# Performance work log

Hardware: AMD Instinct MI355X
Metric: run time of the kernel (lower is better)

Reference implementation:

```python
import jax, jax.numpy as jnp
import numpy as np
import math

T = 1024      # num tokens
D = 1024      # hidden_size
H = 16        # attention heads
KV = 4        # kv heads
DH = 64       # head_dim
E = 8         # routed experts
K = 2         # top-k
F = 512       # moe_intermediate_size
FS = 2048     # shared_expert_intermediate_size
L = 2         # layers
V = 4096      # codec vocab
THETA = 1e6
EPS = 1e-6


def rms(x, w):
    return x * jax.lax.rsqrt(jnp.mean(x * x, -1, keepdims=True) + EPS) * w


def rope(x, pos):
    # x: [T, h, DH], rotate-half (non-interleaved) rotary
    half = DH // 2
    inv = 1.0 / (THETA ** (jnp.arange(half, dtype=jnp.float32) / half))
    ang = pos.astype(jnp.float32)[:, None] * inv          # [T, half]
    cos = jnp.concatenate([jnp.cos(ang)] * 2, -1)[:, None, :]
    sin = jnp.concatenate([jnp.sin(ang)] * 2, -1)[:, None, :]
    rot = jnp.concatenate([-x[..., half:], x[..., :half]], -1)
    return x * cos + rot * sin


def setup_inputs() -> dict:
    key = jax.random.key(0)
    ks = jax.random.split(key, 20)
    s = 0.02
    n = lambda k, shp: jax.random.normal(k, shp, dtype=jnp.float32) * s
    return {
        "input_ids": jax.random.randint(ks[0], (T,), 0, V),
        "positions": jnp.arange(T),
        "emb": n(ks[1], (V, D)),
        "ln1": jnp.ones((L, D), jnp.float32),
        "wq": n(ks[2], (L, D, H * DH)),
        "wk": n(ks[3], (L, D, KV * DH)),
        "wv": n(ks[4], (L, D, KV * DH)),
        "wo": n(ks[5], (L, H * DH, D)),
        "qn": jnp.ones((L, DH), jnp.float32),
        "kn": jnp.ones((L, DH), jnp.float32),
        "ln2": jnp.ones((L, D), jnp.float32),
        "router_w": n(ks[6], (L, D, E)),
        "egu": n(ks[7], (L, E, D, 2 * F)),
        "edn": n(ks[8], (L, E, F, D)),
        "sgu": n(ks[9], (L, D, 2 * FS)),
        "sdn": n(ks[10], (L, FS, D)),
        "sg_gate": n(ks[11], (L, D)),
        "final_ln": jnp.ones((D,), jnp.float32),
    }


def forward(input_ids, positions, emb, ln1, wq, wk, wv, wo, qn, kn, ln2,
            router_w, egu, edn, sgu, sdn, sg_gate, final_ln):
    h = emb[input_ids]                          # [T, D]
    res = jnp.zeros_like(h)
    causal = jnp.tril(jnp.ones((T, T), bool))
    scale = 1.0 / math.sqrt(DH)
    for i in range(L):
        # --- attention (pre-norm, fused add-residual semantics) ---
        res = h + res
        hn = rms(res, ln1[i])
        q = rms((hn @ wq[i]).reshape(T, H, DH), qn[i])
        k = rms((hn @ wk[i]).reshape(T, KV, DH), kn[i])
        v = (hn @ wv[i]).reshape(T, KV, DH)
        q, k = rope(q, positions), rope(k, positions)
        k = jnp.repeat(k, H // KV, axis=1)      # GQA expand
        v = jnp.repeat(v, H // KV, axis=1)
        att = jnp.einsum('qhd,khd->hqk', q, k) * scale
        att = jnp.where(causal[None], att, -jnp.inf)
        att = jax.nn.softmax(att, axis=-1)
        o = jnp.einsum('hqk,khd->qhd', att, v).reshape(T, H * DH) @ wo[i]
        # --- MoE MLP with shared expert ---
        res = o + res
        hn = rms(res, ln2[i])
        # shared expert: SiluAndMul + down, gated by sigmoid scalar
        gu = hn @ sgu[i]
        shared = (jax.nn.silu(gu[:, :FS]) * gu[:, FS:]) @ sdn[i]
        shared = shared * jax.nn.sigmoid(hn @ sg_gate[i])[:, None]
        # routed experts: softmax router, top-k, renormalize
        probs = jax.nn.softmax(hn @ router_w[i], axis=-1)      # [T, E]
        w, idx = jax.lax.top_k(probs, K)
        w = w / jnp.sum(w, -1, keepdims=True)
        comb = jnp.zeros((T, E), hn.dtype).at[jnp.arange(T)[:, None], idx].add(w)
        g = jnp.einsum('td,edf->tef', hn, egu[i])              # [T, E, 2F]
        he = jax.nn.silu(g[..., :F]) * g[..., F:]              # [T, E, F]
        routed = jnp.einsum('tef,efd,te->td', he, edn[i], comb)
        h = routed + shared
    res = h + res
    return rms(res, final_ln)


def reference(input_ids, positions, emb, ln1, wq, wk, wv, wo, qn, kn, ln2,
              router_w, egu, edn, sgu, sdn, sg_gate, final_ln):
    return forward(input_ids, positions, emb, ln1, wq, wk, wv, wo, qn, kn, ln2,
                   router_w, egu, edn, sgu, sdn, sg_gate, final_ln)
```

## Files before the change

kernel.cpp:

```cpp
#include <hip/hip_runtime.h>
#include <hip/hip_bf16.h>

#define T_ 1024
#define D_ 1024
#define H_ 16
#define KV_ 4
#define DH_ 64
#define E_ 8
#define TOPK_ 2
#define F_ 512
#define FS_ 2048
#define L_ 2

typedef unsigned int uint32;
typedef __attribute__((ext_vector_type(8))) short short8;
typedef __attribute__((ext_vector_type(4))) short short4v;
typedef __attribute__((ext_vector_type(4))) float f32x4;

__device__ __forceinline__ short f2bf(float f){
  uint32 u = __float_as_uint(f);
  return (short)((u + 0x7fffu + ((u >> 16) & 1u)) >> 16);
}
__device__ __forceinline__ float bf2f(short s){
  return __uint_as_float(((uint32)(unsigned short)s) << 16);
}

__device__ __forceinline__ void split8(const float* src, short8& h8, short8& l8){
  #pragma unroll
  for (int j = 0; j < 8; j++){
    short hi = f2bf(src[j]);
    h8[j] = hi;
    l8[j] = f2bf(src[j] - bf2f(hi));
  }
}

__global__ void k_embed(const int* __restrict__ ids, const float* __restrict__ emb,
                        float* __restrict__ h, float* __restrict__ res){
  int idx = blockIdx.x * 256 + threadIdx.x;
  int t = idx >> 10, d = idx & 1023;
  h[idx] = emb[(size_t)ids[t] * D_ + d];
  res[idx] = 0.f;
}

__global__ void k_zero_i32(int* __restrict__ p, int n){
  int i = blockIdx.x * 64 + threadIdx.x;
  if (i < n) p[i] = 0;
}

__global__ __launch_bounds__(256)
void k_fused_rms(float* __restrict__ res, const float* __restrict__ h,
                 const float* __restrict__ w, float* __restrict__ out){
  int t = blockIdx.x, tid = threadIdx.x;
  float* rr = res + (size_t)t * D_;
  const float* hr = h + (size_t)t * D_;
  float ss = 0.f;
  float vloc[4];
  #pragma unroll
  for (int u = 0; u < 4; u++){
    int d = tid + u * 256;
    float v = rr[d] + hr[d];
    vloc[u] = v;
    ss += v * v;
  }
  #pragma unroll
  for (int o = 32; o; o >>= 1) ss += __shfl_xor(ss, o);
  __shared__ float red[4];
  if ((tid & 63) == 0) red[tid >> 6] = ss;
  __syncthreads();
  float r = rsqrtf((red[0] + red[1] + red[2] + red[3]) * (1.f / D_) + 1e-6f);
  float* orow = out + (size_t)t * D_;
  #pragma unroll
  for (int u = 0; u < 4; u++){
    int d = tid + u * 256;
    rr[d] = vloc[u];
    orow[d] = vloc[u] * r * w[d];
  }
}

__global__ __launch_bounds__(64)
void k_qknorm_rope(float* __restrict__ buf, const float* __restrict__ nw,
                   const int* __restrict__ pos, int nheads){
  int row = blockIdx.x;
  int t = row / nheads;
  int lane = threadIdx.x;
  int base = row * DH_ + lane;
  float x = buf[base];
  float ss = x * x;
  #pragma unroll
  for (int o = 32; o; o >>= 1) ss += __shfl_xor(ss, o);
  float r = rsqrtf(ss * (1.f / DH_) + 1e-6f);
  float xn = x * r * nw[lane];
  int j = lane & 31;
  float inv = powf(1.0e6f, -(float)j * (1.f / 32.f));
  float ang = (float)pos[t] * inv;
  float s, c;
  sincosf(ang, &s, &c);
  float p = __shfl_xor(xn, 32);
  float rot = (lane < 32) ? -p : p;
  buf[base] = xn * c + rot * s;
}

__global__ __launch_bounds__(256)
void k_fattn(const float* __restrict__ q, const float* __restrict__ k,
             const float* __restrict__ v, float* __restrict__ out){
  const int h = blockIdx.x, qt = blockIdx.y;
  const int kvh = h >> 2;
  const int tid = threadIdx.x;
  const int w = tid >> 6, lane = tid & 63, l16 = lane & 15, lq = lane >> 4;

  __shared__ __align__(16) short Kh[64][72], Kl[64][72];
  __shared__ __align__(16) short Vth[64][72], Vtl[64][72];
  __shared__ __align__(16) short Ph[64][72], Pl[64][72];

  short8 qh[2], ql[2];
  {
    const float* qp = q + ((size_t)(qt * 64 + w * 16 + l16) * H_ + h) * DH_;
    #pragma unroll
    for (int s = 0; s < 2; s++){
      float a8[8];
      *(float4*)&a8[0] = *(const float4*)(qp + lq * 8 + 32 * s);
      *(float4*)&a8[4] = *(const float4*)(qp + lq * 8 + 32 * s + 4);
      split8(a8, qh[s], ql[s]);
    }
  }

  float m_i[4], l_i[4];
  f32x4 acc[4];
  #pragma unroll
  for (int i = 0; i < 4; i++){ m_i[i] = -1e30f; l_i[i] = 0.f; acc[i] = (f32x4){0.f,0.f,0.f,0.f}; }

  const int kc = tid >> 2, kd = (tid & 3) * 16;
  const int vc0 = (tid & 15) * 4, vd0 = (tid >> 4) * 4;
  float kr[16], vr[16];

  {
    const float* kp = k + ((size_t)(0 + kc) * KV_ + kvh) * DH_ + kd;
    #pragma unroll
    for (int u = 0; u < 16; u += 4) *(float4*)&kr[u] = *(const float4*)(kp + u);
    #pragma unroll
    for (int cc = 0; cc < 4; cc++){
      const float* vp = v + ((size_t)(0 + vc0 + cc) * KV_ + kvh) * DH_ + vd0;
      *(float4*)&vr[cc * 4] = *(const float4*)vp;
    }
  }

  for (int kt = 0; kt <= qt; kt++){
    __syncthreads();
    {
      short8 h8, l8;
      split8(&kr[0], h8, l8);
      *(short8*)&Kh[kc][kd] = h8;     *(short8*)&Kl[kc][kd] = l8;
      split8(&kr[8], h8, l8);
      *(short8*)&Kh[kc][kd + 8] = h8; *(short8*)&Kl[kc][kd + 8] = l8;
      #pragma unroll
      for (int dd = 0; dd < 4; dd++){
        short4v hv, lv;
        #pragma unroll
        for (int cc = 0; cc < 4; cc++){
          float f = vr[cc * 4 + dd];
          short hb = f2bf(f);
          hv[cc] = hb;
          lv[cc] = f2bf(f - bf2f(hb));
        }
        *(short4v*)&Vth[vd0 + dd][vc0] = hv;
        *(short4v*)&Vtl[vd0 + dd][vc0] = lv;
      }
    }
    __syncthreads();
    if (kt < qt){
      const float* kp = k + ((size_t)((kt + 1) * 64 + kc) * KV_ + kvh) * DH_ + kd;
      #pragma unroll
      for (int u = 0; u < 16; u += 4) *(float4*)&kr[u] = *(const float4*)(kp + u);
      #pragma unroll
      for (int cc = 0; cc < 4; cc++){
        const float* vp = v + ((size_t)((kt + 1) * 64 + vc0 + cc) * KV_ + kvh) * DH_ + vd0;
        *(float4*)&vr[cc * 4] = *(const float4*)vp;
      }
    }

    f32x4 sa[4];
    #pragma unroll
    for (int ct = 0; ct < 4; ct++) sa[ct] = (f32x4){0.f,0.f,0.f,0.f};
    #pragma unroll
    for (int s = 0; s < 2; s++){
      #pragma unroll
      for (int ct = 0; ct < 4; ct++){
        short8 kh8 = *(const short8*)&Kh[ct * 16 + l16][lq * 8 + 32 * s];
        short8 kl8 = *(const short8*)&Kl[ct * 16 + l16][lq * 8 + 32 * s];
        sa[ct] = __builtin_amdgcn_mfma_f32_16x16x32_bf16(qh[s], kh8, sa[ct], 0, 0, 0);
        sa[ct] = __builtin_amdgcn_mfma_f32_16x16x32_bf16(qh[s], kl8, sa[ct], 0, 0, 0);
        sa[ct] = __builtin_amdgcn_mfma_f32_16x16x32_bf16(ql[s], kh8, sa[ct], 0, 0, 0);
      }
    }

    const bool diag = (kt == qt);
    #pragma unroll
    for (int ct = 0; ct < 4; ct++)
      #pragma unroll
      for (int i = 0; i < 4; i++){
        float sv = sa[ct][i] * 0.125f;
        if (diag && (ct * 16 + l16 > w * 16 + lq * 4 + i)) sv = -1e30f;
        sa[ct][i] = sv;
      }

    #pragma unroll
    for (int i = 0; i < 4; i++){
      float mx = fmaxf(fmaxf(sa[0][i], sa[1][i]), fmaxf(sa[2][i], sa[3][i]));
      #pragma unroll
      for (int o = 8; o; o >>= 1) mx = fmaxf(mx, __shfl_xor(mx, o));
      float mn = fmaxf(m_i[i], mx);
      float al = __expf(m_i[i] - mn);
      float ls = 0.f;
      #pragma unroll
      for (int ct = 0; ct < 4; ct++){
        float pv = __expf(sa[ct][i] - mn);
        sa[ct][i] = pv;
        ls += pv;
      }
      #pragma unroll
      for (int o = 8; o; o >>= 1) ls += __shfl_xor(ls, o);
      l_i[i] = l_i[i] * al + ls;
      m_i[i] = mn;
      #pragma unroll
      for (int dt = 0; dt < 4; dt++) acc[dt][i] *= al;
    }

    {
      int pr = w * 16 + lq * 4;
      #pragma unroll
      for (int i = 0; i < 4; i++)
        #pragma unroll
        for (int ct = 0; ct < 4; ct++){
          float pv = sa[ct][i];
          short hb = f2bf(pv);
          Ph[pr + i][ct * 16 + l16] = hb;
          Pl[pr + i][ct * 16 + l16] = f2bf(pv - bf2f(hb));
        }
    }
    __syncthreads();

    #pragma unroll
    for (int s = 0; s < 2; s++){
      short8 pah = *(const short8*)&Ph[w * 16 + l16][lq * 8 + 32 * s];
      short8 pal = *(const short8*)&Pl[w * 16 + l16][lq * 8 + 32 * s];
      #pragma unroll
      for (int dt = 0; dt < 4; dt++){
        short8 vh8 = *(const short8*)&Vth[dt * 16 + l16][lq * 8 + 32 * s];
        short8 vl8 = *(const short8*)&Vtl[dt * 16 + l16][lq * 8 + 32 * s];
        acc[dt] = __builtin_amdgcn_mfma_f32_16x16x32_bf16(pah, vh8, acc[dt], 0, 0, 0);
        acc[dt] = __builtin_amdgcn_mfma_f32_16x16x32_bf16(pah, vl8, acc[dt], 0, 0, 0);
        acc[dt] = __builtin_amdgcn_mfma_f32_16x16x32_bf16(pal, vh8, acc[dt], 0, 0, 0);
      }
    }
  }

  int orow = qt * 64 + w * 16 + lq * 4;
  #pragma unroll
  for (int i = 0; i < 4; i++){
    float inv = 1.f / l_i[i];
    #pragma unroll
    for (int dt = 0; dt < 4; dt++)
      out[(size_t)(orow + i) * (H_ * DH_) + h * DH_ + dt * 16 + l16] = acc[dt][i] * inv;
  }
}


#define GEMM_LDS  __shared__ __align__(16) short Ah[64][40], Al[64][40], Bh[64][40], Bl[64][40]

__global__ __launch_bounds__(256)
void k_mgemm(const float* __restrict__ A, const float* __restrict__ B,
             float* __restrict__ C, int M, int N, int K){
  GEMM_LDS;
  int tid = threadIdx.x;
  int row0 = blockIdx.y * 64, col0 = blockIdx.x * 64;
  int w = tid >> 6, lane = tid & 63, l16 = lane & 15, lq = lane >> 4;
  int sm = tid & 63, sk = (tid >> 6) * 8;
  bool aok = (row0 + sm) < M;
  const float* Arow = A + (size_t)(row0 + sm) * K + sk;
  const float* Bcol = B + (size_t)sk * N + col0 + sm;
  f32x4 acc[4] = {};
  float a_reg[8], b_reg[8];
  if (aok){
    *(float4*)&a_reg[0] = *(const float4*)(Arow);
    *(float4*)&a_reg[4] = *(const float4*)(Arow + 4);
  } else {
    #pragma unroll
    for (int j = 0; j < 8; j++) a_reg[j] = 0.f;
  }
  #pragma unroll
  for (int j = 0; j < 8; j++) b_reg[j] = Bcol[(size_t)j * N];
  int nc = K >> 5;
  for (int c = 0; c < nc; c++){
    short8 h8, l8;
    split8(a_reg, h8, l8);
    *(short8*)&Ah[sm][sk] = h8;
    *(short8*)&Al[sm][sk] = l8;
    split8(b_reg, h8, l8);
    *(short8*)&Bh[sm][sk] = h8;
    *(short8*)&Bl[sm][sk] = l8;
    __syncthreads();
    if (c + 1 < nc){
      const float* An = Arow + (c + 1) * 32;
      if (aok){
        *(float4*)&a_reg[0] = *(const float4*)(An);
        *(float4*)&a_reg[4] = *(const float4*)(An + 4);
      }
      const float* Bn = Bcol + (size_t)(c + 1) * 32 * N;
      #pragma unroll
      for (int j = 0; j < 8; j++) b_reg[j] = Bn[(size_t)j * N];
    }
    short8 ah = *(const short8*)&Ah[w * 16 + l16][lq * 8];
    short8 al = *(const short8*)&Al[w * 16 + l16][lq * 8];
    #pragma unroll
    for (int nt = 0; nt < 4; nt++){
      short8 bh = *(const short8*)&Bh[nt * 16 + l16][lq * 8];
      short8 bl = *(const short8*)&Bl[nt * 16 + l16][lq * 8];
      acc[nt] = __builtin_amdgcn_mfma_f32_16x16x32_bf16(ah, bh, acc[nt], 0, 0, 0);
      acc[nt] = __builtin_amdgcn_mfma_f32_16x16x32_bf16(ah, bl, acc[nt], 0, 0, 0);
      acc[nt] = __builtin_amdgcn_mfma_f32_16x16x32_bf16(al, bh, acc[nt], 0, 0, 0);
    }
    __syncthreads();
  }
  #pragma unroll
  for (int nt = 0; nt < 4; nt++)
    #pragma unroll
    for (int i = 0; i < 4; i++){
      int r = row0 + w * 16 + lq * 4 + i;
      if (r < M) C[(size_t)r * N + col0 + nt * 16 + l16] = acc[nt][i];
    }
}

__global__ __launch_bounds__(256)
void k_mgemm_up(const float* __restrict__ hn, const float* __restrict__ egu_l,
                float* __restrict__ G, const int* __restrict__ counts,
                const int* __restrict__ offsets, const int* __restrict__ rowtok){
  const int e = blockIdx.z;
  const int me = counts[e];
  const int row0 = blockIdx.y * 64;
  if (row0 >= me) return;
  const int off = offsets[e];
  const float* B = egu_l + (size_t)e * D_ * (2 * F_);
  const int N = 2 * F_, K = D_;
  GEMM_LDS;
  int tid = threadIdx.x;
  int col0 = blockIdx.x * 64;
  int w = tid >> 6, lane = tid & 63, l16 = lane & 15, lq = lane >> 4;
  int sm = tid & 63, sk = (tid >> 6) * 8;
  bool aok = (row0 + sm) < me;
  int tok = aok ? rowtok[off + row0 + sm] : 0;
  const float* Arow = hn + (size_t)tok * K + sk;
  const float* Bcol = B + (size_t)sk * N + col0 + sm;
  f32x4 acc[4] = {};
  float a_reg[8], b_reg[8];
  if (aok){
    *(float4*)&a_reg[0] = *(const float4*)(Arow);
    *(float4*)&a_reg[4] = *(const float4*)(Arow + 4);
  } else {
    #pragma unroll
    for (int j = 0; j < 8; j++) a_reg[j] = 0.f;
  }
  #pragma unroll
  for (int j = 0; j < 8; j++) b_reg[j] = Bcol[(size_t)j * N];
  int nc = K >> 5;
  for (int c = 0; c < nc; c++){
    short8 h8, l8;
    split8(a_reg, h8, l8);
    *(short8*)&Ah[sm][sk] = h8;
    *(short8*)&Al[sm][sk] = l8;
    split8(b_reg, h8, l8);
    *(short8*)&Bh[sm][sk] = h8;
    *(short8*)&Bl[sm][sk] = l8;
    __syncthreads();
    if (c + 1 < nc){
      const float* An = Arow + (c + 1) * 32;
      if (aok){
        *(float4*)&a_reg[0] = *(const float4*)(An);
        *(float4*)&a_reg[4] = *(const float4*)(An + 4);
      }
      const float* Bn = Bcol + (size_t)(c + 1) * 32 * N;
      #pragma unroll
      for (int j = 0; j < 8; j++) b_reg[j] = Bn[(size_t)j * N];
    }
    short8 ah = *(const short8*)&Ah[w * 16 + l16][lq * 8];
    short8 al = *(const short8*)&Al[w * 16 + l16][lq * 8];
    #pragma unroll
    for (int nt = 0; nt < 4; nt++){
      short8 bh = *(const short8*)&Bh[nt * 16 + l16][lq * 8];
      short8 bl = *(const short8*)&Bl[nt * 16 + l16][lq * 8];
      acc[nt] = __builtin_amdgcn_mfma_f32_16x16x32_bf16(ah, bh, acc[nt], 0, 0, 0);
      acc[nt] = __builtin_amdgcn_mfma_f32_16x16x32_bf16(ah, bl, acc[nt], 0, 0, 0);
      acc[nt] = __builtin_amdgcn_mfma_f32_16x16x32_bf16(al, bh, acc[nt], 0, 0, 0);
    }
    __syncthreads();
  }
  #pragma unroll
  for (int nt = 0; nt < 4; nt++)
    #pragma unroll
    for (int i = 0; i < 4; i++){
      int r = row0 + w * 16 + lq * 4 + i;
      if (r < me) G[(size_t)(off + r) * N + col0 + nt * 16 + l16] = acc[nt][i];
    }
}

__global__ __launch_bounds__(256)
void k_mgemm_dn(const float* __restrict__ he, const float* __restrict__ edn_l,
                float* __restrict__ routed, const int* __restrict__ counts,
                const int* __restrict__ offsets, const int* __restrict__ rowtok,
                const float* __restrict__ roww){
  const int e = blockIdx.z;
  const int me = counts[e];
  const int row0 = blockIdx.y * 64;
  if (row0 >= me) return;
  const int off = offsets[e];
  const float* B = edn_l + (size_t)e * F_ * D_;
  const int N = D_, K = F_;
  GEMM_LDS;
  int tid = threadIdx.x;
  int col0 = blockIdx.x * 64;
  int w = tid >> 6, lane = tid & 63, l16 = lane & 15, lq = lane >> 4;
  int sm = tid & 63, sk = (tid >> 6) * 8;
  bool aok = (row0 + sm) < me;
  const float* Arow = he + (size_t)(off + row0 + (aok ? sm : 0)) * K + sk;
  const float* Bcol = B + (size_t)sk * N + col0 + sm;
  f32x4 acc[4] = {};
  float a_reg[8], b_reg[8];
  if (aok){
    *(float4*)&a_reg[0] = *(const float4*)(Arow);
    *(float4*)&a_reg[4] = *(const float4*)(Arow + 4);
  } else {
    #pragma unroll
    for (int j = 0; j < 8; j++) a_reg[j] = 0.f;
  }
  #pragma unroll
  for (int j = 0; j < 8; j++) b_reg[j] = Bcol[(size_t)j * N];
  int nc = K >> 5;
  for (int c = 0; c < nc; c++){
    short8 h8, l8;
    split8(a_reg, h8, l8);
    *(short8*)&Ah[sm][sk] = h8;
    *(short8*)&Al[sm][sk] = l8;
    split8(b_reg, h8, l8);
    *(short8*)&Bh[sm][sk] = h8;
    *(short8*)&Bl[sm][sk] = l8;
    __syncthreads();
    if (c + 1 < nc){
      const float* An = Arow + (c + 1) * 32;
      if (aok){
        *(float4*)&a_reg[0] = *(const float4*)(An);
        *(float4*)&a_reg[4] = *(const float4*)(An + 4);
      }
      const float* Bn = Bcol + (size_t)(c + 1) * 32 * N;
      #pragma unroll
      for (int j = 0; j < 8; j++) b_reg[j] = Bn[(size_t)j * N];
    }
    short8 ah = *(const short8*)&Ah[w * 16 + l16][lq * 8];
    short8 al = *(const short8*)&Al[w * 16 + l16][lq * 8];
    #pragma unroll
    for (int nt = 0; nt < 4; nt++){
      short8 bh = *(const short8*)&Bh[nt * 16 + l16][lq * 8];
      short8 bl = *(const short8*)&Bl[nt * 16 + l16][lq * 8];
      acc[nt] = __builtin_amdgcn_mfma_f32_16x16x32_bf16(ah, bh, acc[nt], 0, 0, 0);
      acc[nt] = __builtin_amdgcn_mfma_f32_16x16x32_bf16(ah, bl, acc[nt], 0, 0, 0);
      acc[nt] = __builtin_amdgcn_mfma_f32_16x16x32_bf16(al, bh, acc[nt], 0, 0, 0);
    }
    __syncthreads();
  }
  #pragma unroll
  for (int i = 0; i < 4; i++){
    int r = row0 + w * 16 + lq * 4 + i;
    if (r < me){
      int tok = rowtok[off + r];
      float wgt = roww[off + r];
      float* cp = routed + (size_t)tok * D_ + col0;
      #pragma unroll
      for (int nt = 0; nt < 4; nt++)
        atomicAdd(&cp[nt * 16 + l16], wgt * acc[nt][i]);
    }
  }
}

__global__ void k_silumul(const float* __restrict__ g, float* __restrict__ out,
                          int width, int half){
  int idx = blockIdx.x * 256 + threadIdx.x;
  int r = idx / half, f = idx - r * half;
  float a = g[(size_t)r * width + f];
  float b = g[(size_t)r * width + half + f];
  out[idx] = a * b / (1.f + __expf(-a));
}

__global__ __launch_bounds__(256)
void k_gate(const float* __restrict__ hn, const float* __restrict__ sg,
            float* __restrict__ gate){
  int t = blockIdx.x, tid = threadIdx.x;
  const float* xr = hn + (size_t)t * D_;
  float s = 0.f;
  for (int d = tid; d < D_; d += 256) s += xr[d] * sg[d];
  #pragma unroll
  for (int o = 32; o; o >>= 1) s += __shfl_xor(s, o);
  __shared__ float red[4];
  if ((tid & 63) == 0) red[tid >> 6] = s;
  __syncthreads();
  if (tid == 0){
    float tot = red[0] + red[1] + red[2] + red[3];
    gate[t] = 1.f / (1.f + __expf(-tot));
  }
}

__global__ __launch_bounds__(64)
void k_router(const float* __restrict__ hn, const float* __restrict__ rw,
              int* __restrict__ counts, int* __restrict__ top_e,
              float* __restrict__ top_w){
  int t = blockIdx.x;
  int lane = threadIdx.x;
  int e = lane & 7, c = lane >> 3;
  const float* xr = hn + (size_t)t * D_;
  float s = 0.f;
  for (int d = c * 128; d < c * 128 + 128; d++) s += xr[d] * rw[d * E_ + e];
  s += __shfl_down(s, 32);
  s += __shfl_down(s, 16);
  s += __shfl_down(s, 8);
  float v[8];
  #pragma unroll
  for (int qq = 0; qq < 8; qq++) v[qq] = __shfl(s, qq);
  if (lane == 0){
    float mx = v[0];
    #pragma unroll
    for (int qq = 1; qq < 8; qq++) mx = fmaxf(mx, v[qq]);
    float p[8];
    #pragma unroll
    for (int qq = 0; qq < 8; qq++) p[qq] = __expf(v[qq] - mx);
    int i0 = 0;
    #pragma unroll
    for (int qq = 1; qq < 8; qq++) if (p[qq] > p[i0]) i0 = qq;
    int i1 = (i0 == 0) ? 1 : 0;
    #pragma unroll
    for (int qq = 0; qq < 8; qq++) if (qq != i0 && p[qq] > p[i1]) i1 = qq;
    float w0 = p[i0], w1 = p[i1];
    float inv = 1.f / (w0 + w1);
    top_e[t * 2 + 0] = i0; top_w[t * 2 + 0] = w0 * inv;
    top_e[t * 2 + 1] = i1; top_w[t * 2 + 1] = w1 * inv;
    atomicAdd(&counts[i0], 1);
    atomicAdd(&counts[i1], 1);
  }
}

__global__ void k_prefix(const int* __restrict__ counts, int* __restrict__ offsets,
                         int* __restrict__ cursor){
  if (threadIdx.x == 0 && blockIdx.x == 0){
    int acc = 0;
    for (int e = 0; e < E_; e++){ offsets[e] = acc; cursor[e] = acc; acc += counts[e]; }
  }
}

__global__ void k_assign(const int* __restrict__ top_e, const float* __restrict__ top_w,
                         int* __restrict__ cursor, int* __restrict__ rowtok,
                         float* __restrict__ roww){
  int i = blockIdx.x * 256 + threadIdx.x;
  if (i >= T_ * TOPK_) return;
  int e = top_e[i];
  int slot = atomicAdd(&cursor[e], 1);
  rowtok[slot] = i >> 1;
  roww[slot] = top_w[i];
}

__global__ void k_prefill(float* __restrict__ h, const float* __restrict__ shexp,
                          const float* __restrict__ gate){
  int idx = blockIdx.x * 256 + threadIdx.x;
  h[idx] = shexp[idx] * gate[idx >> 10];
}

__global__ __launch_bounds__(256)
void k_final_rms(const float* __restrict__ resv, const float* __restrict__ hv,
                 const float* __restrict__ w, float* __restrict__ out){
  int t = blockIdx.x, tid = threadIdx.x;
  const float* xr = resv + (size_t)t * D_;
  const float* hr = hv + (size_t)t * D_;
  float ss = 0.f;
  for (int d = tid; d < D_; d += 256){ float v = xr[d] + hr[d]; ss += v * v; }
  #pragma unroll
  for (int o = 32; o; o >>= 1) ss += __shfl_xor(ss, o);
  __shared__ float red[4];
  if ((tid & 63) == 0) red[tid >> 6] = ss;
  __syncthreads();
  float r = rsqrtf((red[0] + red[1] + red[2] + red[3]) * (1.f / D_) + 1e-6f);
  float* orow = out + (size_t)t * D_;
  for (int d = tid; d < D_; d += 256) orow[d] = (xr[d] + hr[d]) * r * w[d];
}

extern "C" void kernel_launch(void* const* d_in, const int* in_sizes, int n_in,
                              void* d_out, int out_size, void* d_ws, size_t ws_size,
                              hipStream_t stream){
  (void)in_sizes; (void)n_in; (void)out_size; (void)ws_size;
  const int* ids = (const int*)d_in[0];
  const int* pos = (const int*)d_in[1];
  const float* emb = (const float*)d_in[2];
  const float* ln1 = (const float*)d_in[3];
  const float* wq  = (const float*)d_in[4];
  const float* wk  = (const float*)d_in[5];
  const float* wv  = (const float*)d_in[6];
  const float* wo  = (const float*)d_in[7];
  const float* qn  = (const float*)d_in[8];
  const float* kn  = (const float*)d_in[9];
  const float* ln2 = (const float*)d_in[10];
  const float* rw  = (const float*)d_in[11];
  const float* egu = (const float*)d_in[12];
  const float* edn = (const float*)d_in[13];
  const float* sgu = (const float*)d_in[14];
  const float* sdn = (const float*)d_in[15];
  const float* sg  = (const float*)d_in[16];
  const float* fln = (const float*)d_in[17];

  float* ws = (float*)d_ws;
  const size_t MB = (size_t)1 << 20;
  float* res    = ws;
  float* h      = ws + 1 * MB;
  float* hn     = ws + 2 * MB;
  float* qlin   = ws + 3 * MB;
  float* kbuf   = ws + 4 * MB;
  float* vbuf   = kbuf + T_ * KV_ * DH_;
  float* attnb  = ws + 5 * MB;
  float* gu     = ws + 6 * MB;
  float* sact   = ws + 10 * MB;
  float* shexp  = ws + 12 * MB;
  float* G      = ws + 13 * MB;
  float* he     = ws + 15 * MB;
  float* gate   = ws + 17 * MB;
  float* roww   = gate + 4096;
  float* top_w  = roww + 4096;
  int* counts   = (int*)(top_w + 4096);
  int* offsets  = counts + 8;
  int* cursor   = offsets + 8;
  int* top_e    = cursor + 8;
  int* rowtok   = top_e + 2048;

  const int NTD = T_ * D_ / 256;

  k_embed<<<NTD, 256, 0, stream>>>(ids, emb, h, res);

  for (int i = 0; i < L_; i++){
    k_fused_rms<<<T_, 256, 0, stream>>>(res, h, ln1 + (size_t)i * D_, hn);
    k_mgemm<<<dim3(16, 16), 256, 0, stream>>>(hn, wq + (size_t)i * D_ * (H_ * DH_), qlin, T_, H_ * DH_, D_);
    k_mgemm<<<dim3(4, 16), 256, 0, stream>>>(hn, wk + (size_t)i * D_ * (KV_ * DH_), kbuf, T_, KV_ * DH_, D_);
    k_mgemm<<<dim3(4, 16), 256, 0, stream>>>(hn, wv + (size_t)i * D_ * (KV_ * DH_), vbuf, T_, KV_ * DH_, D_);
    k_qknorm_rope<<<T_ * H_, 64, 0, stream>>>(qlin, qn + (size_t)i * DH_, pos, H_);
    k_qknorm_rope<<<T_ * KV_, 64, 0, stream>>>(kbuf, kn + (size_t)i * DH_, pos, KV_);
    k_fattn<<<dim3(H_, T_ / 64), 256, 0, stream>>>(qlin, kbuf, vbuf, attnb);
    k_mgemm<<<dim3(16, 16), 256, 0, stream>>>(attnb, wo + (size_t)i * (H_ * DH_) * D_, h, T_, D_, H_ * DH_);
    k_fused_rms<<<T_, 256, 0, stream>>>(res, h, ln2 + (size_t)i * D_, hn);
    k_mgemm<<<dim3(64, 16), 256, 0, stream>>>(hn, sgu + (size_t)i * D_ * (2 * FS_), gu, T_, 2 * FS_, D_);
    k_silumul<<<T_ * FS_ / 256, 256, 0, stream>>>(gu, sact, 2 * FS_, FS_);
    k_mgemm<<<dim3(16, 16), 256, 0, stream>>>(sact, sdn + (size_t)i * FS_ * D_, shexp, T_, D_, FS_);
    k_gate<<<T_, 256, 0, stream>>>(hn, sg + (size_t)i * D_, gate);
    k_zero_i32<<<1, 64, 0, stream>>>(counts, 8);
    k_router<<<T_, 64, 0, stream>>>(hn, rw + (size_t)i * D_ * E_, counts, top_e, top_w);
    k_prefix<<<1, 1, 0, stream>>>(counts, offsets, cursor);
    k_assign<<<8, 256, 0, stream>>>(top_e, top_w, cursor, rowtok, roww);
    k_mgemm_up<<<dim3(16, 32, 8), 256, 0, stream>>>(hn, egu + (size_t)i * E_ * D_ * (2 * F_), G, counts, offsets, rowtok);
    k_silumul<<<T_ * TOPK_ * F_ / 256, 256, 0, stream>>>(G, he, 2 * F_, F_);
    k_prefill<<<NTD, 256, 0, stream>>>(h, shexp, gate);
    k_mgemm_dn<<<dim3(16, 32, 8), 256, 0, stream>>>(he, edn + (size_t)i * E_ * F_ * D_, h, counts, offsets, rowtok, roww);
  }

  k_final_rms<<<T_, 256, 0, stream>>>(res, h, fln, (float*)d_out);
}
```

Before: 1.132 ms.

## Split K across two partial GEMM slices and fuse QKV projections into one launch

Result: faster. 907.4 us (-19.9%).

```diff
diff --git a/kernel.cpp b/kernel.cpp
--- a/kernel.cpp
+++ b/kernel.cpp
@@ -59,6 +59,38 @@
   for (int u = 0; u < 4; u++){
     int d = tid + u * 256;
     float v = rr[d] + hr[d];
+    vloc[u] = v;
+    ss += v * v;
+  }
+  #pragma unroll
+  for (int o = 32; o; o >>= 1) ss += __shfl_xor(ss, o);
+  __shared__ float red[4];
+  if ((tid & 63) == 0) red[tid >> 6] = ss;
+  __syncthreads();
+  float r = rsqrtf((red[0] + red[1] + red[2] + red[3]) * (1.f / D_) + 1e-6f);
+  float* orow = out + (size_t)t * D_;
+  #pragma unroll
+  for (int u = 0; u < 4; u++){
+    int d = tid + u * 256;
+    rr[d] = vloc[u];
+    orow[d] = vloc[u] * r * w[d];
+  }
+}
+
+__global__ __launch_bounds__(256)
+void k_fused_rms2(float* __restrict__ res, const float* __restrict__ h0,
+                  const float* __restrict__ h1,
+                  const float* __restrict__ w, float* __restrict__ out){
+  int t = blockIdx.x, tid = threadIdx.x;
+  float* rr = res + (size_t)t * D_;
+  const float* h0r = h0 + (size_t)t * D_;
+  const float* h1r = h1 + (size_t)t * D_;
+  float ss = 0.f;
+  float vloc[4];
+  #pragma unroll
+  for (int u = 0; u < 4; u++){
+    int d = tid + u * 256;
+    float v = rr[d] + h0r[d] + h1r[d];
     vloc[u] = v;
     ss += v * v;
   }
@@ -264,63 +296,68 @@
   }
 }
 
-
 #define GEMM_LDS  __shared__ __align__(16) short Ah[64][40], Al[64][40], Bh[64][40], Bl[64][40]
+
+#define GEMM_BODY(APTR, KFULL, KBASE, KH, BPTR, N_, MROW_OK)                                  \
+  f32x4 acc[4] = {};                                                                          \
+  {                                                                                           \
+    int tid = threadIdx.x;                                                                    \
+    int w_ = tid >> 6, lane = tid & 63, l16 = lane & 15, lq = lane >> 4;                      \
+    int sm = tid & 63, sk = (tid >> 6) * 8;                                                   \
+    (void)w_; (void)l16; (void)lq;                                                            \
+    const float* Arow = (APTR) + (size_t)(KBASE) + sk;                                        \
+    const float* Bcol = (BPTR) + (size_t)((KBASE) + sk) * (N_) + col0 + sm;                   \
+    float a_reg[8], b_reg[8];                                                                 \
+    if (MROW_OK){                                                                             \
+      *(float4*)&a_reg[0] = *(const float4*)(Arow);                                           \
+      *(float4*)&a_reg[4] = *(const float4*)(Arow + 4);                                       \
+    } else {                                                                                  \
+      _Pragma("unroll") for (int j = 0; j < 8; j++) a_reg[j] = 0.f;                           \
+    }                                                                                         \
+    _Pragma("unroll") for (int j = 0; j < 8; j++) b_reg[j] = Bcol[(size_t)j * (N_)];          \
+    int nc = (KH) >> 5;                                                                       \
+    for (int c = 0; c < nc; c++){                                                             \
+      short8 h8, l8;                                                                          \
+      split8(a_reg, h8, l8);                                                                  \
+      *(short8*)&Ah[sm][sk] = h8;                                                             \
+      *(short8*)&Al[sm][sk] = l8;                                                             \
+      split8(b_reg, h8, l8);                                                                  \
+      *(short8*)&Bh[sm][sk] = h8;                                                             \
+      *(short8*)&Bl[sm][sk] = l8;                                                             \
+      __syncthreads();                                                                        \
+      if (c + 1 < nc){                                                                        \
+        const float* An = Arow + (c + 1) * 32;                                                \
+        if (MROW_OK){                                                                         \
+          *(float4*)&a_reg[0] = *(const float4*)(An);                                         \
+          *(float4*)&a_reg[4] = *(const float4*)(An + 4);                                     \
+        }                                                                                     \
+        const float* Bn = Bcol + (size_t)(c + 1) * 32 * (N_);                                 \
+        _Pragma("unroll") for (int j = 0; j < 8; j++) b_reg[j] = Bn[(size_t)j * (N_)];        \
+      }                                                                                       \
+      short8 ah = *(const short8*)&Ah[w_ * 16 + l16][lq * 8];                                 \
+      short8 al = *(const short8*)&Al[w_ * 16 + l16][lq * 8];                                 \
+      _Pragma("unroll")                                                                       \
+      for (int nt = 0; nt < 4; nt++){                                                         \
+        short8 bh = *(const short8*)&Bh[nt * 16 + l16][lq * 8];                               \
+        short8 bl = *(const short8*)&Bl[nt * 16 + l16][lq * 8];                               \
+        acc[nt] = __builtin_amdgcn_mfma_f32_16x16x32_bf16(ah, bh, acc[nt], 0, 0, 0);          \
+        acc[nt] = __builtin_amdgcn_mfma_f32_16x16x32_bf16(ah, bl, acc[nt], 0, 0, 0);          \
+        acc[nt] = __builtin_amdgcn_mfma_f32_16x16x32_bf16(al, bh, acc[nt], 0, 0, 0);          \
+      }                                                                                       \
+      __syncthreads();                                                                        \
+    }                                                                                         \
+  }
 
 __global__ __launch_bounds__(256)
 void k_mgemm(const float* __restrict__ A, const float* __restrict__ B,
              float* __restrict__ C, int M, int N, int K){
   GEMM_LDS;
-  int tid = threadIdx.x;
   int row0 = blockIdx.y * 64, col0 = blockIdx.x * 64;
-  int w = tid >> 6, lane = tid & 63, l16 = lane & 15, lq = lane >> 4;
-  int sm = tid & 63, sk = (tid >> 6) * 8;
+  int sm = threadIdx.x & 63;
   bool aok = (row0 + sm) < M;
-  const float* Arow = A + (size_t)(row0 + sm) * K + sk;
-  const float* Bcol = B + (size_t)sk * N + col0 + sm;
-  f32x4 acc[4] = {};
-  float a_reg[8], b_reg[8];
-  if (aok){
-    *(float4*)&a_reg[0] = *(const float4*)(Arow);
-    *(float4*)&a_reg[4] = *(const float4*)(Arow + 4);
-  } else {
-    #pragma unroll
-    for (int j = 0; j < 8; j++) a_reg[j] = 0.f;
-  }
-  #pragma unroll
-  for (int j = 0; j < 8; j++) b_reg[j] = Bcol[(size_t)j * N];
-  int nc = K >> 5;
-  for (int c = 0; c < nc; c++){
-    short8 h8, l8;
-    split8(a_reg, h8, l8);
-    *(short8*)&Ah[sm][sk] = h8;
-    *(short8*)&Al[sm][sk] = l8;
-    split8(b_reg, h8, l8);
-    *(short8*)&Bh[sm][sk] = h8;
-    *(short8*)&Bl[sm][sk] = l8;
-    __syncthreads();
-    if (c + 1 < nc){
-      const float* An = Arow + (c + 1) * 32;
-      if (aok){
-        *(float4*)&a_reg[0] = *(const float4*)(An);
-        *(float4*)&a_reg[4] = *(const float4*)(An + 4);
-      }
-      const float* Bn = Bcol + (size_t)(c + 1) * 32 * N;
-      #pragma unroll
-      for (int j = 0; j < 8; j++) b_reg[j] = Bn[(size_t)j * N];
-    }
-    short8 ah = *(const short8*)&Ah[w * 16 + l16][lq * 8];
-    short8 al = *(const short8*)&Al[w * 16 + l16][lq * 8];
-    #pragma unroll
-    for (int nt = 0; nt < 4; nt++){
-      short8 bh = *(const short8*)&Bh[nt * 16 + l16][lq * 8];
-      short8 bl = *(const short8*)&Bl[nt * 16 + l16][lq * 8];
-      acc[nt] = __builtin_amdgcn_mfma_f32_16x16x32_bf16(ah, bh, acc[nt], 0, 0, 0);
-      acc[nt] = __builtin_amdgcn_mfma_f32_16x16x32_bf16(ah, bl, acc[nt], 0, 0, 0);
-      acc[nt] = __builtin_amdgcn_mfma_f32_16x16x32_bf16(al, bh, acc[nt], 0, 0, 0);
-    }
-    __syncthreads();
-  }
+  const float* Abase = A + (size_t)(row0 + sm) * K;
+  GEMM_BODY(Abase, K, 0, K, B, N, aok);
+  int w = threadIdx.x >> 6, lane = threadIdx.x & 63, l16 = lane & 15, lq = lane >> 4;
   #pragma unroll
   for (int nt = 0; nt < 4; nt++)
     #pragma unroll
@@ -331,68 +368,74 @@
 }
 
 __global__ __launch_bounds__(256)
+void k_mgemm_ks2(const float* __restrict__ A, const float* __restrict__ B,
+                 float* __restrict__ C0, float* __restrict__ C1,
+                 int M, int N, int K){
+  GEMM_LDS;
+  int row0 = blockIdx.y * 64, col0 = blockIdx.x * 64;
+  int z = blockIdx.z, KH = K >> 1;
+  int sm = threadIdx.x & 63;
+  bool aok = (row0 + sm) < M;
+  const float* Abase = A + (size_t)(row0 + sm) * K;
+  GEMM_BODY(Abase, K, z * KH, KH, B, N, aok);
+  float* C = z ? C1 : C0;
+  int w = threadIdx.x >> 6, lane = threadIdx.x & 63, l16 = lane & 15, lq = lane >> 4;
+  #pragma unroll
+  for (int nt = 0; nt < 4; nt++)
+    #pragma unroll
+    for (int i = 0; i < 4; i++){
+      int r = row0 + w * 16 + lq * 4 + i;
+      if (r < M) C[(size_t)r * N + col0 + nt * 16 + l16] = acc[nt][i];
+    }
+}
+
+__global__ __launch_bounds__(256)
+void k_mgemm_qkv(const float* __restrict__ hn, const float* __restrict__ wq_l,
+                 const float* __restrict__ wk_l, const float* __restrict__ wv_l,
+                 float* __restrict__ qlin, float* __restrict__ kbuf,
+                 float* __restrict__ vbuf){
+  GEMM_LDS;
+  int cb = blockIdx.x;
+  const float* B; float* C; int N; int col0;
+  if (cb < 16){ B = wq_l; C = qlin; N = H_ * DH_; col0 = cb * 64; }
+  else if (cb < 20){ B = wk_l; C = kbuf; N = KV_ * DH_; col0 = (cb - 16) * 64; }
+  else { B = wv_l; C = vbuf; N = KV_ * DH_; col0 = (cb - 20) * 64; }
+  int row0 = blockIdx.y * 64;
+  int sm = threadIdx.x & 63;
+  const float* Abase = hn + (size_t)(row0 + sm) * D_;
+  GEMM_BODY(Abase, D_, 0, D_, B, N, true);
+  int w = threadIdx.x >> 6, lane = threadIdx.x & 63, l16 = lane & 15, lq = lane >> 4;
+  #pragma unroll
+  for (int nt = 0; nt < 4; nt++)
+    #pragma unroll
+    for (int i = 0; i < 4; i++){
+      int r = row0 + w * 16 + lq * 4 + i;
+      C[(size_t)r * N + col0 + nt * 16 + l16] = acc[nt][i];
+    }
+}
+
+__global__ __launch_bounds__(256)
 void k_mgemm_up(const float* __restrict__ hn, const float* __restrict__ egu_l,
-                float* __restrict__ G, const int* __restrict__ counts,
-                const int* __restrict__ offsets, const int* __restrict__ rowtok){
-  const int e = blockIdx.z;
+                float* __restrict__ G0, float* __restrict__ G1,
+                const int* __restrict__ counts, const int* __restrict__ offsets,
+                const int* __restrict__ rowtok){
+  const int z = blockIdx.z;
+  const int e = z >> 1, s = z & 1;
   const int me = counts[e];
   const int row0 = blockIdx.y * 64;
   if (row0 >= me) return;
   const int off = offsets[e];
   const float* B = egu_l + (size_t)e * D_ * (2 * F_);
-  const int N = 2 * F_, K = D_;
+  const int N = 2 * F_, KH = D_ >> 1;
   GEMM_LDS;
-  int tid = threadIdx.x;
   int col0 = blockIdx.x * 64;
-  int w = tid >> 6, lane = tid & 63, l16 = lane & 15, lq = lane >> 4;
-  int sm = tid & 63, sk = (tid >> 6) * 8;
+  int sm = threadIdx.x & 63;
   bool aok = (row0 + sm) < me;
   int tok = aok ? rowtok[off + row0 + sm] : 0;
-  const float* Arow = hn + (size_t)tok * K + sk;
-  const float* Bcol = B + (size_t)sk * N + col0 + sm;
-  f32x4 acc[4] = {};
-  float a_reg[8], b_reg[8];
-  if (aok){
-    *(float4*)&a_reg[0] = *(const float4*)(Arow);
-    *(float4*)&a_reg[4] = *(const float4*)(Arow + 4);
-  } else {
-    #pragma unroll
-    for (int j = 0; j < 8; j++) a_reg[j] = 0.f;
-  }
-  #pragma unroll
-  for (int j = 0; j < 8; j++) b_reg[j] = Bcol[(size_t)j * N];
-  int nc = K >> 5;
-  for (int c = 0; c < nc; c++){
-    short8 h8, l8;
-    split8(a_reg, h8, l8);
-    *(short8*)&Ah[sm][sk] = h8;
-    *(short8*)&Al[sm][sk] = l8;
-    split8(b_reg, h8, l8);
-    *(short8*)&Bh[sm][sk] = h8;
-    *(short8*)&Bl[sm][sk] = l8;
-    __syncthreads();
-    if (c + 1 < nc){
-      const float* An = Arow + (c + 1) * 32;
-      if (aok){
-        *(float4*)&a_reg[0] = *(const float4*)(An);
-        *(float4*)&a_reg[4] = *(const float4*)(An + 4);
-      }
-      const float* Bn = Bcol + (size_t)(c + 1) * 32 * N;
-      #pragma unroll
-      for (int j = 0; j < 8; j++) b_reg[j] = Bn[(size_t)j * N];
-    }
-    short8 ah = *(const short8*)&Ah[w * 16 + l16][lq * 8];
-    short8 al = *(const short8*)&Al[w * 16 + l16][lq * 8];
-    #pragma unroll
-    for (int nt = 0; nt < 4; nt++){
-      short8 bh = *(const short8*)&Bh[nt * 16 + l16][lq * 8];
-      short8 bl = *(const short8*)&Bl[nt * 16 + l16][lq * 8];
-      acc[nt] = __builtin_amdgcn_mfma_f32_16x16x32_bf16(ah, bh, acc[nt], 0, 0, 0);
-      acc[nt] = __builtin_amdgcn_mfma_f32_16x16x32_bf16(ah, bl, acc[nt], 0, 0, 0);
-      acc[nt] = __builtin_amdgcn_mfma_f32_16x16x32_bf16(al, bh, acc[nt], 0, 0, 0);
-    }
-    __syncthreads();
-  }
+  const float* Abase = hn + (size_t)tok * D_;
+  GEMM_BODY(Abase, D_, s * KH, KH, B, N, aok);
+  float* G = s ? G1 : G0;
+  int w = threadIdx.x >> 6, lane = threadIdx.x & 63, l16 = lane & 15, lq = lane >> 4;
   #pragma unroll
   for (int nt = 0; nt < 4; nt++)
     #pragma unroll
@@ -407,64 +450,21 @@
                 float* __restrict__ routed, const int* __restrict__ counts,
                 const int* __restrict__ offsets, const int* __restrict__ rowtok,
                 const float* __restrict__ roww){
-  const int e = blockIdx.z;
+  const int z = blockIdx.z;
+  const int e = z >> 1, s = z & 1;
   const int me = counts[e];
   const int row0 = blockIdx.y * 64;
   if (row0 >= me) return;
   const int off = offsets[e];
   const float* B = edn_l + (size_t)e * F_ * D_;
-  const int N = D_, K = F_;
+  const int N = D_, KH = F_ >> 1;
   GEMM_LDS;
-  int tid = threadIdx.x;
   int col0 = blockIdx.x * 64;
-  int w = tid >> 6, lane = tid & 63, l16 = lane & 15, lq = lane >> 4;
-  int sm = tid & 63, sk = (tid >> 6) * 8;
+  int sm = threadIdx.x & 63;
   bool aok = (row0 + sm) < me;
-  const float* Arow = he + (size_t)(off + row0 + (aok ? sm : 0)) * K + sk;
-  const float* Bcol = B + (size_t)sk * N + col0 + sm;
-  f32x4 acc[4] = {};
-  float a_reg[8], b_reg[8];
-  if (aok){
-    *(float4*)&a_reg[0] = *(const float4*)(Arow);
-    *(float4*)&a_reg[4] = *(const float4*)(Arow + 4);
-  } else {
-    #pragma unroll
-    for (int j = 0; j < 8; j++) a_reg[j] = 0.f;
-  }
-  #pragma unroll
-  for (int j = 0; j < 8; j++) b_reg[j] = Bcol[(size_t)j * N];
-  int nc = K >> 5;
-  for (int c = 0; c < nc; c++){
-    short8 h8, l8;
-    split8(a_reg, h8, l8);
-    *(short8*)&Ah[sm][sk] = h8;
-    *(short8*)&Al[sm][sk] = l8;
-    split8(b_reg, h8, l8);
-    *(short8*)&Bh[sm][sk] = h8;
-    *(short8*)&Bl[sm][sk] = l8;
-    __syncthreads();
-    if (c + 1 < nc){
-      const float* An = Arow + (c + 1) * 32;
-      if (aok){
-        *(float4*)&a_reg[0] = *(const float4*)(An);
-        *(float4*)&a_reg[4] = *(const float4*)(An + 4);
-      }
-      const float* Bn = Bcol + (size_t)(c + 1) * 32 * N;
-      #pragma unroll
-      for (int j = 0; j < 8; j++) b_reg[j] = Bn[(size_t)j * N];
-    }
-    short8 ah = *(const short8*)&Ah[w * 16 + l16][lq * 8];
-    short8 al = *(const short8*)&Al[w * 16 + l16][lq * 8];
-    #pragma unroll
-    for (int nt = 0; nt < 4; nt++){
-      short8 bh = *(const short8*)&Bh[nt * 16 + l16][lq * 8];
-      short8 bl = *(const short8*)&Bl[nt * 16 + l16][lq * 8];
-      acc[nt] = __builtin_amdgcn_mfma_f32_16x16x32_bf16(ah, bh, acc[nt], 0, 0, 0);
-      acc[nt] = __builtin_amdgcn_mfma_f32_16x16x32_bf16(ah, bl, acc[nt], 0, 0, 0);
-      acc[nt] = __builtin_amdgcn_mfma_f32_16x16x32_bf16(al, bh, acc[nt], 0, 0, 0);
-    }
-    __syncthreads();
-  }
+  const float* Abase = he + (size_t)(off + row0 + (aok ? sm : 0)) * F_;
+  GEMM_BODY(Abase, F_, s * KH, KH, B, N, aok);
+  int w = threadIdx.x >> 6, lane = threadIdx.x & 63, l16 = lane & 15, lq = lane >> 4;
   #pragma unroll
   for (int i = 0; i < 4; i++){
     int r = row0 + w * 16 + lq * 4 + i;
@@ -485,6 +485,16 @@
   int r = idx / half, f = idx - r * half;
   float a = g[(size_t)r * width + f];
   float b = g[(size_t)r * width + half + f];
+  out[idx] = a * b / (1.f + __expf(-a));
+}
+
+__global__ void k_silumul2(const float* __restrict__ g0, const float* __restrict__ g1,
+                           float* __restrict__ out, int width, int half){
+  int idx = blockIdx.x * 256 + threadIdx.x;
+  int r = idx / half, f = idx - r * half;
+  size_t ia = (size_t)r * width + f, ib = (size_t)r * width + half + f;
+  float a = g0[ia] + g1[ia];
+  float b = g0[ib] + g1[ib];
   out[idx] = a * b / (1.f + __expf(-a));
 }
 
@@ -563,10 +573,10 @@
   roww[slot] = top_w[i];
 }
 
-__global__ void k_prefill(float* __restrict__ h, const float* __restrict__ shexp,
-                          const float* __restrict__ gate){
+__global__ void k_prefill2(float* __restrict__ h, const float* __restrict__ p0,
+                           const float* __restrict__ p1, const float* __restrict__ gate){
   int idx = blockIdx.x * 256 + threadIdx.x;
-  h[idx] = shexp[idx] * gate[idx >> 10];
+  h[idx] = (p0[idx] + p1[idx]) * gate[idx >> 10];
 }
 
 __global__ __launch_bounds__(256)
@@ -621,9 +631,10 @@
   float* attnb  = ws + 5 * MB;
   float* gu     = ws + 6 * MB;
   float* sact   = ws + 10 * MB;
-  float* shexp  = ws + 12 * MB;
-  float* G      = ws + 13 * MB;
+  float* ps0    = ws + 12 * MB;
+  float* G0     = ws + 13 * MB;
   float* he     = ws + 15 * MB;
+  float* ps1    = ws + 16 * MB;
   float* gate   = ws + 17 * MB;
   float* roww   = gate + 4096;
   float* top_w  = roww + 4096;
@@ -632,6 +643,9 @@
   int* cursor   = offsets + 8;
   int* top_e    = cursor + 8;
   int* rowtok   = top_e + 2048;
+  float* G1     = ws + 3 * MB;
+  float* pw0    = ws + 3 * MB;
+  float* pw1    = ws + 4 * MB;
 
   const int NTD = T_ * D_ / 256;
 
@@ -639,26 +653,30 @@
 
   for (int i = 0; i < L_; i++){
     k_fused_rms<<<T_, 256, 0, stream>>>(res, h, ln1 + (size_t)i * D_, hn);
-    k_mgemm<<<dim3(16, 16), 256, 0, stream>>>(hn, wq + (size_t)i * D_ * (H_ * DH_), qlin, T_, H_ * DH_, D_);
-    k_mgemm<<<dim3(4, 16), 256, 0, stream>>>(hn, wk + (size_t)i * D_ * (KV_ * DH_), kbuf, T_, KV_ * DH_, D_);
-    k_mgemm<<<dim3(4, 16), 256, 0, stream>>>(hn, wv + (size_t)i * D_ * (KV_ * DH_), vbuf, T_, KV_ * DH_, D_);
+    k_mgemm_qkv<<<dim3(24, 16), 256, 0, stream>>>(hn,
+        wq + (size_t)i * D_ * (H_ * DH_), wk + (size_t)i * D_ * (KV_ * DH_),
+        wv + (size_t)i * D_ * (KV_ * DH_), qlin, kbuf, vbuf);
     k_qknorm_rope<<<T_ * H_, 64, 0, stream>>>(qlin, qn + (size_t)i * DH_, pos, H_);
     k_qknorm_rope<<<T_ * KV_, 64, 0, stream>>>(kbuf, kn + (size_t)i * DH_, pos, KV_);
     k_fattn<<<dim3(H_, T_ / 64), 256, 0, stream>>>(qlin, kbuf, vbuf, attnb);
-    k_mgemm<<<dim3(16, 16), 256, 0, stream>>>(attnb, wo + (size_t)i * (H_ * DH_) * D_, h, T_, D_, H_ * DH_);
-    k_fused_rms<<<T_, 256, 0, stream>>>(res, h, ln2 + (size_t)i * D_, hn);
+    k_mgemm_ks2<<<dim3(16, 16, 2), 256, 0, stream>>>(attnb, wo + (size_t)i * (H_ * DH_) * D_,
+                                                     pw0, pw1, T_, D_, H_ * DH_);
+    k_fused_rms2<<<T_, 256, 0, stream>>>(res, pw0, pw1, ln2 + (size_t)i * D_, hn);
     k_mgemm<<<dim3(64, 16), 256, 0, stream>>>(hn, sgu + (size_t)i * D_ * (2 * FS_), gu, T_, 2 * FS_, D_);
     k_silumul<<<T_ * FS_ / 256, 256, 0, stream>>>(gu, sact, 2 * FS_, FS_);
-    k_mgemm<<<dim3(16, 16), 256, 0, stream>>>(sact, sdn + (size_t)i * FS_ * D_, shexp, T_, D_, FS_);
+    k_mgemm_ks2<<<dim3(16, 16, 2), 256, 0, stream>>>(sact, sdn + (size_t)i * FS_ * D_,
+                                                     ps0, ps1, T_, D_, FS_);
     k_gate<<<T_, 256, 0, stream>>>(hn, sg + (size_t)i * D_, gate);
     k_zero_i32<<<1, 64, 0, stream>>>(counts, 8);
     k_router<<<T_, 64, 0, stream>>>(hn, rw + (size_t)i * D_ * E_, counts, top_e, top_w);
     k_prefix<<<1, 1, 0, stream>>>(counts, offsets, cursor);
     k_assign<<<8, 256, 0, stream>>>(top_e, top_w, cursor, rowtok, roww);
-    k_mgemm_up<<<dim3(16, 32, 8), 256, 0, stream>>>(hn, egu + (size_t)i * E_ * D_ * (2 * F_), G, counts, offsets, rowtok);
-    k_silumul<<<T_ * TOPK_ * F_ / 256, 256, 0, stream>>>(G, he, 2 * F_, F_);
-    k_prefill<<<NTD, 256, 0, stream>>>(h, shexp, gate);
-    k_mgemm_dn<<<dim3(16, 32, 8), 256, 0, stream>>>(he, edn + (size_t)i * E_ * F_ * D_, h, counts, offsets, rowtok, roww);
+    k_mgemm_up<<<dim3(16, 32, 16), 256, 0, stream>>>(hn, egu + (size_t)i * E_ * D_ * (2 * F_),
+                                                     G0, G1, counts, offsets, rowtok);
+    k_silumul2<<<T_ * TOPK_ * F_ / 256, 256, 0, stream>>>(G0, G1, he, 2 * F_, F_);
+    k_prefill2<<<NTD, 256, 0, stream>>>(h, ps0, ps1, gate);
+    k_mgemm_dn<<<dim3(16, 32, 16), 256, 0, stream>>>(he, edn + (size_t)i * E_ * F_ * D_,
+                                                     h, counts, offsets, rowtok, roww);
   }
 
   k_final_rms<<<T_, 256, 0, stream>>>(res, h, fln, (float*)d_out);
```
